# Optimization experiments

Hardware: AMD Instinct MI355X
Metric: run time of the kernel (lower is better)

Reference implementation:

```python
import jax, jax.numpy as jnp
import numpy as np

ITERATION = 10

def setup_inputs() -> dict:
    key = jax.random.key(0)
    k1, k2, k3 = jax.random.split(key, 3)
    a_inter = jax.random.normal(k1, (8, 64, 64, 32, 32), dtype=jnp.float32)
    logits = jax.random.normal(k2, (8, 64), dtype=jnp.float32)
    W = jax.random.normal(k3, (1, 64, 64), dtype=jnp.float32)
    return {"a_inter": a_inter, "logits": logits, "W": W}


def reference(a_inter, logits, W):
    N = W.shape[1]  # num_nodes
    B = a_inter.shape[0]
    # feats: [B, N, C*H*W]
    feats = a_inter[:, :, :N, :, :].reshape(B, N, -1)
    # expand logits [B, N] -> [B, N, N] (unsqueeze(1).expand in torch)
    logits0 = jnp.broadcast_to(logits[:, None, :], (B, N, N))

    feats_norm = jnp.linalg.norm(feats, ord=2, axis=2, keepdims=True)  # [B, N, 1]
    pairwise_norm = feats_norm @ jnp.swapaxes(feats_norm, 1, 2)        # [B, N, N]
    pairwise_dot = feats @ jnp.swapaxes(feats, 1, 2)                   # [B, N, N]
    pairwise_sim = pairwise_dot / (pairwise_norm + 1e-6)
    W_sym = (W + jnp.swapaxes(W, 1, 2)) / 2.0
    pairwise_potential = pairwise_sim * W_sym                          # [B, N, N]

    unary_potential = logits0

    def body(i, l):
        probs = jnp.swapaxes(jax.nn.sigmoid(l), 1, 2)  # [B, N, N]
        # probs*pp - (1-probs)*pp == (2*probs - 1)*pp
        pp_E = jnp.sum((2.0 * probs - 1.0) * pairwise_potential, axis=2, keepdims=True)
        return unary_potential + pp_E

    logits_out = jax.lax.fori_loop(0, ITERATION, body, logits0)
    return logits_out.mean(axis=1)  # [B, N]
```

## Files before the change

kernel.cpp:

```cpp
#include <hip/hip_runtime.h>
#include <math.h>

#define BATCH 8
#define NN 64
#define DD 65536
#define BPB 64
#define NBLK (BATCH * BPB)
#define KC (DD / BPB)
#define KW (KC / 4)
#define KSTEPS (KW / 32)

typedef float  floatx4 __attribute__((ext_vector_type(4)));
typedef __bf16 bf16x8  __attribute__((ext_vector_type(8)));

static __device__ __forceinline__ bf16x8 cvt8(float4 lo, float4 hi) {
    const unsigned sel = 0x07060302u;
    union { unsigned u[4]; bf16x8 v; } r;
    r.u[0] = __builtin_amdgcn_perm(__float_as_uint(lo.y), __float_as_uint(lo.x), sel);
    r.u[1] = __builtin_amdgcn_perm(__float_as_uint(lo.w), __float_as_uint(lo.z), sel);
    r.u[2] = __builtin_amdgcn_perm(__float_as_uint(hi.y), __float_as_uint(hi.x), sel);
    r.u[3] = __builtin_amdgcn_perm(__float_as_uint(hi.w), __float_as_uint(hi.z), sel);
    return r.v;
}

__global__ __launch_bounds__(256) void gram_partial_kernel(const float* __restrict__ a,
                                                           float* __restrict__ part) {
    __shared__ __align__(16) float red[3][16][64][4];

    const int bid = blockIdx.x;
    const int b = bid >> 6;
    const int c = bid & (BPB - 1);

    const int tid  = threadIdx.x;
    const int w    = tid >> 6;
    const int lane = tid & 63;
    const int m    = lane & 15;
    const int q    = lane >> 4;

    const float* base = a + (size_t)b * NN * DD + (size_t)c * KC + (size_t)w * KW
                          + (size_t)m * DD + q * 8;
    const float* p0 = base;
    const float* p1 = base + (size_t)16 * DD;
    const float* p2 = base + (size_t)32 * DD;
    const float* p3 = base + (size_t)48 * DD;

    floatx4 acc[16];
    #pragma unroll
    for (int i = 0; i < 16; ++i) acc[i] = (floatx4)0.0f;

    float4 A0, A1, A2, A3, A4, A5, A6, A7;
    float4 B0, B1, B2, B3, B4, B5, B6, B7;

#define LOADSET(R0,R1,R2,R3,R4,R5,R6,R7, o)                                \
    R0 = *(const float4*)(p0 + (o));  R1 = *(const float4*)(p0 + (o) + 4); \
    R2 = *(const float4*)(p1 + (o));  R3 = *(const float4*)(p1 + (o) + 4); \
    R4 = *(const float4*)(p2 + (o));  R5 = *(const float4*)(p2 + (o) + 4); \
    R6 = *(const float4*)(p3 + (o));  R7 = *(const float4*)(p3 + (o) + 4);

#define MFMASET(R0,R1,R2,R3,R4,R5,R6,R7)                                   \
    {                                                                      \
        bf16x8 f0 = cvt8(R0, R1);                                          \
        bf16x8 f1 = cvt8(R2, R3);                                          \
        bf16x8 f2 = cvt8(R4, R5);                                          \
        bf16x8 f3 = cvt8(R6, R7);                                          \
        acc[ 0] = __builtin_amdgcn_mfma_f32_16x16x32_bf16(f0, f0, acc[ 0], 0, 0, 0); \
        acc[ 1] = __builtin_amdgcn_mfma_f32_16x16x32_bf16(f0, f1, acc[ 1], 0, 0, 0); \
        acc[ 2] = __builtin_amdgcn_mfma_f32_16x16x32_bf16(f0, f2, acc[ 2], 0, 0, 0); \
        acc[ 3] = __builtin_amdgcn_mfma_f32_16x16x32_bf16(f0, f3, acc[ 3], 0, 0, 0); \
        acc[ 4] = __builtin_amdgcn_mfma_f32_16x16x32_bf16(f1, f0, acc[ 4], 0, 0, 0); \
        acc[ 5] = __builtin_amdgcn_mfma_f32_16x16x32_bf16(f1, f1, acc[ 5], 0, 0, 0); \
        acc[ 6] = __builtin_amdgcn_mfma_f32_16x16x32_bf16(f1, f2, acc[ 6], 0, 0, 0); \
        acc[ 7] = __builtin_amdgcn_mfma_f32_16x16x32_bf16(f1, f3, acc[ 7], 0, 0, 0); \
        acc[ 8] = __builtin_amdgcn_mfma_f32_16x16x32_bf16(f2, f0, acc[ 8], 0, 0, 0); \
        acc[ 9] = __builtin_amdgcn_mfma_f32_16x16x32_bf16(f2, f1, acc[ 9], 0, 0, 0); \
        acc[10] = __builtin_amdgcn_mfma_f32_16x16x32_bf16(f2, f2, acc[10], 0, 0, 0); \
        acc[11] = __builtin_amdgcn_mfma_f32_16x16x32_bf16(f2, f3, acc[11], 0, 0, 0); \
        acc[12] = __builtin_amdgcn_mfma_f32_16x16x32_bf16(f3, f0, acc[12], 0, 0, 0); \
        acc[13] = __builtin_amdgcn_mfma_f32_16x16x32_bf16(f3, f1, acc[13], 0, 0, 0); \
        acc[14] = __builtin_amdgcn_mfma_f32_16x16x32_bf16(f3, f2, acc[14], 0, 0, 0); \
        acc[15] = __builtin_amdgcn_mfma_f32_16x16x32_bf16(f3, f3, acc[15], 0, 0, 0); \
    }

    LOADSET(A0,A1,A2,A3,A4,A5,A6,A7, 0)
    #pragma unroll
    for (int s = 0; s < KSTEPS; s += 2) {
        LOADSET(B0,B1,B2,B3,B4,B5,B6,B7, (s + 1) * 32)
        MFMASET(A0,A1,A2,A3,A4,A5,A6,A7)
        if (s + 2 < KSTEPS) { LOADSET(A0,A1,A2,A3,A4,A5,A6,A7, (s + 2) * 32) }
        MFMASET(B0,B1,B2,B3,B4,B5,B6,B7)
    }
#undef LOADSET
#undef MFMASET

    if (w > 0) {
        #pragma unroll
        for (int t = 0; t < 16; ++t)
            *(floatx4*)&red[w - 1][t][lane][0] = acc[t];
    }
    __syncthreads();
    if (w == 0) {
        #pragma unroll
        for (int t = 0; t < 16; ++t) {
            floatx4 r0 = *(const floatx4*)&red[0][t][lane][0];
            floatx4 r1 = *(const floatx4*)&red[1][t][lane][0];
            floatx4 r2 = *(const floatx4*)&red[2][t][lane][0];
            acc[t] += (r0 + r1) + r2;
        }
        float* pg = part + (size_t)bid * (NN * NN);
        #pragma unroll
        for (int t = 0; t < 16; ++t) {
            float* tp = pg + t * 256 + m;
            #pragma unroll
            for (int r = 0; r < 4; ++r)
                tp[(q * 4 + r) * 16] = acc[t][r];
        }
    }
}

__global__ __launch_bounds__(128) void gram_reduce_kernel(const float* __restrict__ part,
                                                          float* __restrict__ gram) {
    const int gid = blockIdx.x * 128 + threadIdx.x;
    const int b   = gid >> 12;
    const int idx = gid & 4095;
    const int i   = idx >> 6;
    const int j   = idx & 63;
    const int off = ((i >> 4) * 4 + (j >> 4)) * 256 + (i & 15) * 16 + (j & 15);
    const float* p = part + (size_t)b * BPB * (NN * NN) + off;

    float s0 = 0.f, s1 = 0.f, s2 = 0.f, s3 = 0.f;
    #pragma unroll 4
    for (int c = 0; c < BPB; c += 4) {
        s0 += p[(size_t)(c + 0) * (NN * NN)];
        s1 += p[(size_t)(c + 1) * (NN * NN)];
        s2 += p[(size_t)(c + 2) * (NN * NN)];
        s3 += p[(size_t)(c + 3) * (NN * NN)];
    }
    gram[gid] = (s0 + s1) + (s2 + s3);
}

__global__ __launch_bounds__(256) void crf_kernel(const float* __restrict__ gram,
                                                  const float* __restrict__ logits,
                                                  const float* __restrict__ Wm,
                                                  float* __restrict__ out) {
    __shared__ float pp[NN][NN + 1];
    __shared__ float E[NN];
    __shared__ float nrm[NN];
    __shared__ float part[4 * NN];

    const int b  = blockIdx.x;
    const int tid = threadIdx.x;
    const int i  = tid & 63;
    const int jq = tid >> 6;
    const float* g = gram + b * NN * NN;

    if (jq == 0) nrm[i] = sqrtf(g[i * NN + i]);
    E[i] = 0.0f;
    __syncthreads();

    const float ni = nrm[i];
    for (int jj = 0; jj < 16; ++jj) {
        int j = jq * 16 + jj;
        float wsym = 0.5f * (Wm[i * NN + j] + Wm[j * NN + i]);
        pp[i][j] = g[i * NN + j] / (ni * nrm[j] + 1e-6f) * wsym;
    }
    const float li = logits[b * NN + i];
    __syncthreads();

    for (int it = 0; it < 10; ++it) {
        float acc = 0.0f;
        for (int jj = 0; jj < 16; ++jj) {
            int j = jq * 16 + jj;
            float t = li + E[j];
            float s = 1.0f / (1.0f + expf(-t));
            acc = fmaf(2.0f * s - 1.0f, pp[i][j], acc);
        }
        part[jq * NN + i] = acc;
        __syncthreads();
        if (jq == 0)
            E[i] = part[i] + part[NN + i] + part[2 * NN + i] + part[3 * NN + i];
        __syncthreads();
    }

    if (tid < 64) {
        float s = E[tid];
        for (int off = 32; off > 0; off >>= 1) s += __shfl_down(s, off);
        float meanE = __shfl(s, 0) * (1.0f / 64.0f);
        out[b * NN + tid] = logits[b * NN + tid] + meanE;
    }
}

extern "C" void kernel_launch(void* const* d_in, const int* in_sizes, int n_in,
                              void* d_out, int out_size, void* d_ws, size_t ws_size,
                              hipStream_t stream) {
    const float* a      = (const float*)d_in[0];
    const float* logits = (const float*)d_in[1];
    const float* Wm     = (const float*)d_in[2];
    float* out  = (float*)d_out;

    float* part = (float*)d_ws;
    float* gram = part + (size_t)NBLK * NN * NN;

    gram_partial_kernel<<<NBLK, 256, 0, stream>>>(a, part);
    gram_reduce_kernel<<<(BATCH * NN * NN) / 128, 128, 0, stream>>>(part, gram);
    crf_kernel<<<BATCH, 256, 0, stream>>>(gram, logits, Wm, out);
}
```

Baseline: 224.3 us.

## Exploit Gram matrix symmetry: compute only upper-triangular 16x16 tiles

The partial Gram kernel now computes only the 10 upper-triangular 16x16 tile blocks instead of all 16, using symmetry of feats·featsᵀ. The reduce kernel maps lower-triangle entries to their transposed location in the smaller partial buffer. This cuts MFMA work, accumulator registers, LDS reduction and partial-buffer traffic. Launch bounds add a minimum of 3 blocks per SM to raise occupancy now that fewer registers are needed. The main kernel is likely bound by reading 128MB of input, so the gain may be limited.

```diff
diff --git a/kernel.cpp b/kernel.cpp
--- a/kernel.cpp
+++ b/kernel.cpp
@@ -9,6 +9,8 @@
 #define KC (DD / BPB)
 #define KW (KC / 4)
 #define KSTEPS (KW / 32)
+#define NTRI 10
+#define PSZ (NTRI * 256)
 
 typedef float  floatx4 __attribute__((ext_vector_type(4)));
 typedef __bf16 bf16x8  __attribute__((ext_vector_type(8)));
@@ -23,9 +25,9 @@
     return r.v;
 }
 
-__global__ __launch_bounds__(256) void gram_partial_kernel(const float* __restrict__ a,
-                                                           float* __restrict__ part) {
-    __shared__ __align__(16) float red[3][16][64][4];
+__global__ __launch_bounds__(256, 3) void gram_partial_kernel(const float* __restrict__ a,
+                                                              float* __restrict__ part) {
+    __shared__ __align__(16) float red[3][NTRI][64][4];
 
     const int bid = blockIdx.x;
     const int b = bid >> 6;
@@ -44,9 +46,9 @@
     const float* p2 = base + (size_t)32 * DD;
     const float* p3 = base + (size_t)48 * DD;
 
-    floatx4 acc[16];
+    floatx4 acc[NTRI];
     #pragma unroll
-    for (int i = 0; i < 16; ++i) acc[i] = (floatx4)0.0f;
+    for (int i = 0; i < NTRI; ++i) acc[i] = (floatx4)0.0f;
 
     float4 A0, A1, A2, A3, A4, A5, A6, A7;
     float4 B0, B1, B2, B3, B4, B5, B6, B7;
@@ -63,22 +65,16 @@
         bf16x8 f1 = cvt8(R2, R3);                                          \
         bf16x8 f2 = cvt8(R4, R5);                                          \
         bf16x8 f3 = cvt8(R6, R7);                                          \
-        acc[ 0] = __builtin_amdgcn_mfma_f32_16x16x32_bf16(f0, f0, acc[ 0], 0, 0, 0); \
-        acc[ 1] = __builtin_amdgcn_mfma_f32_16x16x32_bf16(f0, f1, acc[ 1], 0, 0, 0); \
-        acc[ 2] = __builtin_amdgcn_mfma_f32_16x16x32_bf16(f0, f2, acc[ 2], 0, 0, 0); \
-        acc[ 3] = __builtin_amdgcn_mfma_f32_16x16x32_bf16(f0, f3, acc[ 3], 0, 0, 0); \
-        acc[ 4] = __builtin_amdgcn_mfma_f32_16x16x32_bf16(f1, f0, acc[ 4], 0, 0, 0); \
-        acc[ 5] = __builtin_amdgcn_mfma_f32_16x16x32_bf16(f1, f1, acc[ 5], 0, 0, 0); \
-        acc[ 6] = __builtin_amdgcn_mfma_f32_16x16x32_bf16(f1, f2, acc[ 6], 0, 0, 0); \
-        acc[ 7] = __builtin_amdgcn_mfma_f32_16x16x32_bf16(f1, f3, acc[ 7], 0, 0, 0); \
-        acc[ 8] = __builtin_amdgcn_mfma_f32_16x16x32_bf16(f2, f0, acc[ 8], 0, 0, 0); \
-        acc[ 9] = __builtin_amdgcn_mfma_f32_16x16x32_bf16(f2, f1, acc[ 9], 0, 0, 0); \
-        acc[10] = __builtin_amdgcn_mfma_f32_16x16x32_bf16(f2, f2, acc[10], 0, 0, 0); \
-        acc[11] = __builtin_amdgcn_mfma_f32_16x16x32_bf16(f2, f3, acc[11], 0, 0, 0); \
-        acc[12] = __builtin_amdgcn_mfma_f32_16x16x32_bf16(f3, f0, acc[12], 0, 0, 0); \
-        acc[13] = __builtin_amdgcn_mfma_f32_16x16x32_bf16(f3, f1, acc[13], 0, 0, 0); \
-        acc[14] = __builtin_amdgcn_mfma_f32_16x16x32_bf16(f3, f2, acc[14], 0, 0, 0); \
-        acc[15] = __builtin_amdgcn_mfma_f32_16x16x32_bf16(f3, f3, acc[15], 0, 0, 0); \
+        acc[0] = __builtin_amdgcn_mfma_f32_16x16x32_bf16(f0, f0, acc[0], 0, 0, 0); \
+        acc[1] = __builtin_amdgcn_mfma_f32_16x16x32_bf16(f0, f1, acc[1], 0, 0, 0); \
+        acc[2] = __builtin_amdgcn_mfma_f32_16x16x32_bf16(f0, f2, acc[2], 0, 0, 0); \
+        acc[3] = __builtin_amdgcn_mfma_f32_16x16x32_bf16(f0, f3, acc[3], 0, 0, 0); \
+        acc[4] = __builtin_amdgcn_mfma_f32_16x16x32_bf16(f1, f1, acc[4], 0, 0, 0); \
+        acc[5] = __builtin_amdgcn_mfma_f32_16x16x32_bf16(f1, f2, acc[5], 0, 0, 0); \
+        acc[6] = __builtin_amdgcn_mfma_f32_16x16x32_bf16(f1, f3, acc[6], 0, 0, 0); \
+        acc[7] = __builtin_amdgcn_mfma_f32_16x16x32_bf16(f2, f2, acc[7], 0, 0, 0); \
+        acc[8] = __builtin_amdgcn_mfma_f32_16x16x32_bf16(f2, f3, acc[8], 0, 0, 0); \
+        acc[9] = __builtin_amdgcn_mfma_f32_16x16x32_bf16(f3, f3, acc[9], 0, 0, 0); \
     }
 
     LOADSET(A0,A1,A2,A3,A4,A5,A6,A7, 0)
@@ -94,21 +90,21 @@
 
     if (w > 0) {
         #pragma unroll
-        for (int t = 0; t < 16; ++t)
+        for (int t = 0; t < NTRI; ++t)
             *(floatx4*)&red[w - 1][t][lane][0] = acc[t];
     }
     __syncthreads();
     if (w == 0) {
         #pragma unroll
-        for (int t = 0; t < 16; ++t) {
+        for (int t = 0; t < NTRI; ++t) {
             floatx4 r0 = *(const floatx4*)&red[0][t][lane][0];
             floatx4 r1 = *(const floatx4*)&red[1][t][lane][0];
             floatx4 r2 = *(const floatx4*)&red[2][t][lane][0];
             acc[t] += (r0 + r1) + r2;
         }
-        float* pg = part + (size_t)bid * (NN * NN);
+        float* pg = part + (size_t)bid * PSZ;
         #pragma unroll
-        for (int t = 0; t < 16; ++t) {
+        for (int t = 0; t < NTRI; ++t) {
             float* tp = pg + t * 256 + m;
             #pragma unroll
             for (int r = 0; r < 4; ++r)
@@ -124,16 +120,22 @@
     const int idx = gid & 4095;
     const int i   = idx >> 6;
     const int j   = idx & 63;
-    const int off = ((i >> 4) * 4 + (j >> 4)) * 256 + (i & 15) * 16 + (j & 15);
-    const float* p = part + (size_t)b * BPB * (NN * NN) + off;
+    const int ti  = i >> 4, tj = j >> 4;
+    const int ib  = ti <= tj ? ti : tj;
+    const int jb  = ti <= tj ? tj : ti;
+    const int slot = ib * 4 - (ib * (ib - 1)) / 2 + (jb - ib);
+    const int rr  = (ti <= tj) ? (i & 15) : (j & 15);
+    const int cc  = (ti <= tj) ? (j & 15) : (i & 15);
+    const int off = slot * 256 + rr * 16 + cc;
+    const float* p = part + (size_t)b * BPB * PSZ + off;
 
     float s0 = 0.f, s1 = 0.f, s2 = 0.f, s3 = 0.f;
     #pragma unroll 4
     for (int c = 0; c < BPB; c += 4) {
-        s0 += p[(size_t)(c + 0) * (NN * NN)];
-        s1 += p[(size_t)(c + 1) * (NN * NN)];
-        s2 += p[(size_t)(c + 2) * (NN * NN)];
-        s3 += p[(size_t)(c + 3) * (NN * NN)];
+        s0 += p[(size_t)(c + 0) * PSZ];
+        s1 += p[(size_t)(c + 1) * PSZ];
+        s2 += p[(size_t)(c + 2) * PSZ];
+        s3 += p[(size_t)(c + 3) * PSZ];
     }
     gram[gid] = (s0 + s1) + (s2 + s3);
 }
@@ -198,7 +200,7 @@
     float* out  = (float*)d_out;
 
     float* part = (float*)d_ws;
-    float* gram = part + (size_t)NBLK * NN * NN;
+    float* gram = part + (size_t)NBLK * PSZ;
 
     gram_partial_kernel<<<NBLK, 256, 0, stream>>>(a, part);
     gram_reduce_kernel<<<(BATCH * NN * NN) / 128, 128, 0, stream>>>(part, gram);
```

Measured after the change: 217.8 us. -2.9%, faster.
